# Optimization experiments

Hardware: AMD Instinct MI355X
Metric: run time of the kernel (lower is better)

## Reference

```python
import jax, jax.numpy as jnp
import numpy as np

B, D, H, W_ = 2, 256, 64, 64


def setup_inputs() -> dict:
    key = jax.random.key(0)
    k1, k2 = jax.random.split(key)
    x = jax.random.normal(k1, (B, D, H, W_), dtype=jnp.float32)
    W = jax.random.normal(k2, (3 * D, D), dtype=jnp.float32) * 0.02  # 1x1 conv weight [out,in]
    b = jnp.zeros((3 * D,), dtype=jnp.float32)
    return {"x": x, "W": W, "b": b}


def reference(x, W, b):
    Bs, d, h, w = x.shape
    N = h * w
    sqrtV = d ** 0.25  # sqrt(sqrt(d)); q,k each divided -> qk^T / sqrt(d)
    # 1x1 conv == per-pixel linear over channels
    qkv = jnp.einsum('bchw,oc->bohw', x, W) + b[None, :, None, None]
    q, k, v = jnp.split(qkv, 3, axis=1)
    q = q.reshape(Bs, d, N).transpose(0, 2, 1) / sqrtV  # [B,N,d]
    k = k.reshape(Bs, d, N).transpose(0, 2, 1) / sqrtV
    v = v.reshape(Bs, d, N).transpose(0, 2, 1)
    # Sinkhorn (eps=1, max_iter=1, uniform marginals 1/N), log domain.
    # cost C = -q k^T  =>  -C = q k^T (softmax-style logits)
    negC = jnp.einsum('bnd,bmd->bnm', q, k)  # [B,N,N]
    logm = jnp.log(1.0 / N + 1e-8).astype(x.dtype)
    u = logm - jax.nn.logsumexp(negC, axis=-1)            # [B,N] row update
    vpot = logm - jax.nn.logsumexp(negC + u[..., None], axis=-2)  # [B,N] col update
    pi = jnp.exp(negC + u[..., None] + vpot[:, None, :])  # transport plan = attn
    out = jnp.einsum('bnm,bmd->bnd', pi, v)               # [B,N,d]
    return out.transpose(0, 2, 1).reshape(Bs, d, h, w)
```

## Files before the change

### kernel.cpp

```cpp
#include <hip/hip_runtime.h>
#include <hip/hip_bf16.h>
#include <math.h>

typedef __bf16 bf16;
typedef __bf16 bf16x8 __attribute__((ext_vector_type(8)));
typedef __bf16 bf16x4 __attribute__((ext_vector_type(4)));
typedef float floatx4 __attribute__((ext_vector_type(4)));

typedef const __attribute__((address_space(1))) void* gas_t;
typedef __attribute__((address_space(3))) void* las_t;

#define NPIX 4096
#define DCH 256
#define LSTR 72

#define OFF_XB   ((size_t)0)
#define OFF_WB   ((size_t)4194304)
#define OFF_Q    ((size_t)4587520)
#define OFF_K    ((size_t)8781824)
#define OFF_V    ((size_t)12976128)
#define OFF_E    ((size_t)17170432)
#define OFF_VPP  ((size_t)84279296)
#define OFF_PART ((size_t)88473600)
#define OFF_RS   ((size_t)122028032)
#define OFF_CS   ((size_t)122060800)

__device__ __forceinline__ void stage_tile(const bf16* __restrict__ g0, size_t rstride,
                                           bf16* lds, int t) {
  const int wbase = (t >> 6) << 6;
#pragma unroll
  for (int i = 0; i < 4; i++) {
    int slot = i * 256 + t;
    int row = slot >> 3, seg = slot & 7;
    const bf16* g = g0 + (size_t)row * rstride + ((seg ^ (row & 7)) << 3);
    bf16* l = lds + (size_t)(i * 256 + wbase) * 8;
    __builtin_amdgcn_global_load_lds((gas_t)g, (las_t)l, 16, 0, 0);
  }
}

__global__ __launch_bounds__(256) void transpose_x(
    const float* __restrict__ x, bf16* __restrict__ xb)
{
  __shared__ float ts[64][65];
  const int t = threadIdx.x;
  const int b = blockIdx.z, n0 = blockIdx.x * 64, c0 = blockIdx.y * 64;
  const float* xp = x + ((size_t)b * DCH + c0) * NPIX + n0;
  for (int i = 0; i < 4; i++) {
    int slot = t + i * 256;
    int c = slot >> 4, nq = (slot & 15) * 4;
    float4 v = *(const float4*)(xp + (size_t)c * NPIX + nq);
    ts[c][nq + 0] = v.x; ts[c][nq + 1] = v.y; ts[c][nq + 2] = v.z; ts[c][nq + 3] = v.w;
  }
  __syncthreads();
  for (int i = 0; i < 2; i++) {
    int slot = t + i * 256;
    int n = slot >> 3, cq = (slot & 7) * 8;
    bf16x8 pk;
    for (int j = 0; j < 8; j++) pk[j] = (bf16)ts[cq + j][n];
    *(bf16x8*)(xb + ((size_t)b * NPIX + n0 + n) * DCH + c0 + cq) = pk;
  }
}

__global__ __launch_bounds__(256) void convert_w(
    const float* __restrict__ W, bf16* __restrict__ wb)
{
  size_t i = ((size_t)blockIdx.x * 256 + threadIdx.x) * 4;
  float4 v = *(const float4*)(W + i);
  bf16x4 pk = { (bf16)v.x, (bf16)v.y, (bf16)v.z, (bf16)v.w };
  *(bf16x4*)(wb + i) = pk;
}

__global__ __launch_bounds__(256) void conv_mfma(
    const bf16* __restrict__ xb, const bf16* __restrict__ wb,
    const float* __restrict__ bias,
    bf16* __restrict__ qb, bf16* __restrict__ kb, bf16* __restrict__ vb)
{
  __shared__ bf16 at[128 * 64];
  __shared__ bf16 bt[128 * 64];
  __shared__ float bs[128];
  const int t  = threadIdx.x;
  const int n0 = blockIdx.x * 128;
  const int o0 = blockIdx.y * 128;
  if (t < 128) bs[t] = bias[o0 + t];
  const int lane = t & 63, wave = t >> 6;
  const int wm = wave >> 1, wn = wave & 1;
  const int l15 = lane & 15, quad = lane >> 4;
  const int l7 = l15 & 7;

  floatx4 acc[4][4];
  for (int i=0;i<4;i++) for (int j=0;j<4;j++) for (int r=0;r<4;r++) acc[i][j][r] = 0.f;

  for (int k0 = 0; k0 < DCH; k0 += 64) {
    stage_tile(wb + (size_t)o0 * DCH + k0, DCH, at, t);
    stage_tile(xb + (size_t)n0 * DCH + k0, DCH, bt, t);
    __syncthreads();
    for (int kk = 0; kk < 2; kk++) {
      bf16x8 af[4], bfr[4];
      int sw = ((kk * 4 + quad) ^ l7) * 8;
      for (int f = 0; f < 4; f++)
        af[f]  = *(const bf16x8*)&at[(wm*64 + f*16 + l15)*64 + sw];
      for (int f = 0; f < 4; f++)
        bfr[f] = *(const bf16x8*)&bt[(wn*64 + f*16 + l15)*64 + sw];
      for (int fm = 0; fm < 4; fm++)
        for (int fn = 0; fn < 4; fn++)
          acc[fm][fn] = __builtin_amdgcn_mfma_f32_16x16x32_bf16(af[fm], bfr[fn], acc[fm][fn], 0, 0, 0);
    }
    __syncthreads();
  }

  const float scale = (o0 < 512) ? 0.25f : 1.0f;
  bf16* dst; int od;
  if (o0 < 256)      { dst = qb; od = o0; }
  else if (o0 < 512) { dst = kb; od = o0 - 256; }
  else               { dst = vb; od = o0 - 512; }

  for (int fm = 0; fm < 4; fm++)
    for (int fn = 0; fn < 4; fn++) {
      int o_l = wm*64 + fm*16 + quad*4;
      int n_g = n0 + wn*64 + fn*16 + l15;
      bf16x4 pk;
      for (int r = 0; r < 4; r++)
        pk[r] = (bf16)((acc[fm][fn][r] + bs[o_l + r]) * scale);
      *(bf16x4*)(dst + (size_t)n_g * DCH + od + o_l) = pk;
    }
}

__global__ __launch_bounds__(256) void pass_a(
    const bf16* __restrict__ qb, const bf16* __restrict__ kb,
    bf16* __restrict__ E, float* __restrict__ rowsum)
{
  __shared__ bf16 kt[128 * 64];
  __shared__ bf16 qt[128 * 64];
  __shared__ float rowpart[128];
  const int b = blockIdx.z;
  qb += (size_t)b * NPIX * DCH;
  kb += (size_t)b * NPIX * DCH;
  E  += (size_t)b * NPIX * NPIX;
  rowsum += b * NPIX;
  const int t  = threadIdx.x;
  const int m0 = blockIdx.x * 128;
  const int n0 = blockIdx.y * 128;
  const int lane = t & 63, wave = t >> 6;
  const int wm = wave >> 1, wn = wave & 1;
  const int l15 = lane & 15, quad = lane >> 4;
  const int l7 = l15 & 7;

  floatx4 acc[4][4];
  for (int i=0;i<4;i++) for (int j=0;j<4;j++) for (int r=0;r<4;r++) acc[i][j][r] = 0.f;

  for (int k0 = 0; k0 < DCH; k0 += 64) {
    stage_tile(kb + (size_t)m0 * DCH + k0, DCH, kt, t);
    stage_tile(qb + (size_t)n0 * DCH + k0, DCH, qt, t);
    __syncthreads();
    for (int kk = 0; kk < 2; kk++) {
      bf16x8 af[4], bfr[4];
      int sw = ((kk * 4 + quad) ^ l7) * 8;
      for (int f = 0; f < 4; f++)
        af[f]  = *(const bf16x8*)&kt[(wm*64 + f*16 + l15)*64 + sw];
      for (int f = 0; f < 4; f++)
        bfr[f] = *(const bf16x8*)&qt[(wn*64 + f*16 + l15)*64 + sw];
      for (int fm = 0; fm < 4; fm++)
        for (int fn = 0; fn < 4; fn++)
          acc[fm][fn] = __builtin_amdgcn_mfma_f32_16x16x32_bf16(af[fm], bfr[fn], acc[fm][fn], 0, 0, 0);
    }
    __syncthreads();
  }

  if (t < 128) rowpart[t] = 0.f;
  __syncthreads();

  float rsum[4] = {0.f, 0.f, 0.f, 0.f};
  for (int fm = 0; fm < 4; fm++)
    for (int fn = 0; fn < 4; fn++) {
      int n_g = n0 + wn*64 + fn*16 + l15;
      int m_g = m0 + wm*64 + fm*16 + quad*4;
      bf16x4 pk;
      float s = 0.f;
      for (int r = 0; r < 4; r++) {
        float e = __expf(acc[fm][fn][r]);
        pk[r] = (bf16)e;
        s += e;
      }
      *(bf16x4*)(E + (size_t)n_g * NPIX + m_g) = pk;
      rsum[fn] += s;
    }
  for (int fn = 0; fn < 4; fn++) {
    float s = rsum[fn];
    s += __shfl_xor(s, 16);
    s += __shfl_xor(s, 32);
    if (quad == 0) atomicAdd(&rowpart[wn*64 + fn*16 + l15], s);
  }
  __syncthreads();
  if (t < 128) atomicAdd(&rowsum[n0 + t], rowpart[t]);
}

__global__ __launch_bounds__(256) void col_pass(
    const bf16* __restrict__ E, const float* __restrict__ rowsum,
    float* __restrict__ colsum, float logm)
{
  __shared__ float eus[32];
  const int b = blockIdx.z;
  E += (size_t)b * NPIX * NPIX;
  rowsum += b * NPIX;
  colsum += b * NPIX;
  const int t = threadIdx.x;
  const int col = blockIdx.x * 1024 + t * 4;
  const int nbase = blockIdx.y * 32;
  if (t < 32) eus[t] = __expf(logm - __logf(rowsum[nbase + t]));
  __syncthreads();
  float acc[4] = {0.f, 0.f, 0.f, 0.f};
  for (int r = 0; r < 32; r++) {
    float eu = eus[r];
    bf16x4 ev = *(const bf16x4*)(E + (size_t)(nbase + r) * NPIX + col);
    for (int i = 0; i < 4; i++) acc[i] += eu * (float)ev[i];
  }
  for (int i = 0; i < 4; i++) atomicAdd(&colsum[col + i], acc[i]);
}

__global__ __launch_bounds__(256) void vpp_kernel(
    const bf16* __restrict__ vb, const float* __restrict__ colsum,
    bf16* __restrict__ vppT, float logm)
{
  __shared__ float ts[64][65];
  __shared__ float ef[64];
  const int b = blockIdx.z;
  vb += (size_t)b * NPIX * DCH;
  colsum += b * NPIX;
  vppT += (size_t)b * DCH * NPIX;
  const int t = threadIdx.x;
  const int m0 = blockIdx.x * 64, d0 = blockIdx.y * 64;
  if (t < 64) ef[t] = __expf(logm - __logf(colsum[m0 + t]));
  __syncthreads();
  for (int i = 0; i < 2; i++) {
    int slot = t + i * 256;
    int m = slot >> 3, dq = (slot & 7) * 8;
    bf16x8 v = *(const bf16x8*)(vb + (size_t)(m0 + m) * DCH + d0 + dq);
    float s = ef[m];
    for (int j = 0; j < 8; j++) ts[dq + j][m] = s * (float)v[j];
  }
  __syncthreads();
  for (int i = 0; i < 2; i++) {
    int slot = t + i * 256;
    int d = slot >> 3, mq = (slot & 7) * 8;
    bf16x8 pk;
    for (int j = 0; j < 8; j++) pk[j] = (bf16)ts[d][mq + j];
    *(bf16x8*)(vppT + (size_t)(d0 + d) * NPIX + m0 + mq) = pk;
  }
}

__global__ __launch_bounds__(256) void pass_c(
    const bf16* __restrict__ E, const bf16* __restrict__ vppT,
    const float* __restrict__ rowsum, float* __restrict__ part, float logm)
{
  __shared__ bf16 et[128 * 64];
  __shared__ bf16 vt[128 * 64];
  __shared__ float eus[128];
  const int z = blockIdx.z;
  const int b = z >> 2, kc = z & 3;
  E += (size_t)b * NPIX * NPIX;
  vppT += (size_t)b * DCH * NPIX;
  rowsum += b * NPIX;
  part += (size_t)(b * 4 + kc) * DCH * NPIX;
  const int t  = threadIdx.x;
  const int n0 = blockIdx.x * 128;
  const int d0 = blockIdx.y * 128;
  const int mstart = kc * 1024;
  if (t < 128) eus[t] = __expf(logm - __logf(rowsum[n0 + t]));
  const int lane = t & 63, wave = t >> 6;
  const int wn = wave >> 1, wd = wave & 1;
  const int l15 = lane & 15, quad = lane >> 4;
  const int l7 = l15 & 7;

  floatx4 acc[4][4];
  for (int i=0;i<4;i++) for (int j=0;j<4;j++) for (int r=0;r<4;r++) acc[i][j][r] = 0.f;
  __syncthreads();

  for (int k0 = mstart; k0 < mstart + 1024; k0 += 64) {
    stage_tile(E + (size_t)n0 * NPIX + k0, NPIX, et, t);
    stage_tile(vppT + (size_t)d0 * NPIX + k0, NPIX, vt, t);
    __syncthreads();
    for (int kk = 0; kk < 2; kk++) {
      bf16x8 af[4], bfr[4];
      int sw = ((kk * 4 + quad) ^ l7) * 8;
      for (int f = 0; f < 4; f++)
        af[f]  = *(const bf16x8*)&et[(wn*64 + f*16 + l15)*64 + sw];
      for (int f = 0; f < 4; f++)
        bfr[f] = *(const bf16x8*)&vt[(wd*64 + f*16 + l15)*64 + sw];
      for (int fn = 0; fn < 4; fn++)
        for (int fd = 0; fd < 4; fd++)
          acc[fn][fd] = __builtin_amdgcn_mfma_f32_16x16x32_bf16(af[fn], bfr[fd], acc[fn][fd], 0, 0, 0);
    }
    __syncthreads();
  }

  for (int fn = 0; fn < 4; fn++)
    for (int fd = 0; fd < 4; fd++) {
      int d_g = d0 + wd*64 + fd*16 + l15;
      int n_l = wn*64 + fn*16 + quad*4;
      float4 o;
      o.x = acc[fn][fd][0] * eus[n_l + 0];
      o.y = acc[fn][fd][1] * eus[n_l + 1];
      o.z = acc[fn][fd][2] * eus[n_l + 2];
      o.w = acc[fn][fd][3] * eus[n_l + 3];
      *(float4*)(part + (size_t)d_g * NPIX + n0 + n_l) = o;
    }
}

__global__ __launch_bounds__(256) void reduce_k(
    const float* __restrict__ part, float* __restrict__ outp)
{
  size_t i4 = ((size_t)blockIdx.x * 256 + threadIdx.x) * 4;
  size_t b = i4 >> 20;
  size_t off = i4 & (size_t)1048575;
  const float* p = part + b * 4 * (size_t)1048576 + off;
  float4 a = *(const float4*)(p);
  float4 bq = *(const float4*)(p + (size_t)1048576);
  float4 c = *(const float4*)(p + (size_t)2097152);
  float4 d = *(const float4*)(p + (size_t)3145728);
  float4 s = { a.x+bq.x+c.x+d.x, a.y+bq.y+c.y+d.y, a.z+bq.z+c.z+d.z, a.w+bq.w+c.w+d.w };
  *(float4*)(outp + i4) = s;
}

extern "C" void kernel_launch(void* const* d_in, const int* in_sizes, int n_in,
                              void* d_out, int out_size, void* d_ws, size_t ws_size,
                              hipStream_t stream) {
  (void)in_sizes; (void)n_in; (void)out_size; (void)ws_size;
  const float* x    = (const float*)d_in[0];
  const float* Wm   = (const float*)d_in[1];
  const float* bias = (const float*)d_in[2];
  float* outp = (float*)d_out;
  char* ws = (char*)d_ws;

  bf16*  xb   = (bf16*)(ws + OFF_XB);
  bf16*  wb   = (bf16*)(ws + OFF_WB);
  bf16*  qb   = (bf16*)(ws + OFF_Q);
  bf16*  kb   = (bf16*)(ws + OFF_K);
  bf16*  vb   = (bf16*)(ws + OFF_V);
  bf16*  E    = (bf16*)(ws + OFF_E);
  bf16*  vppT = (bf16*)(ws + OFF_VPP);
  float* part = (float*)(ws + OFF_PART);
  float* rs   = (float*)(ws + OFF_RS);
  float* cs   = (float*)(ws + OFF_CS);

  const float logm = logf(1.0f / 4096.0f + 1e-8f);

  hipMemsetAsync(ws + OFF_RS, 0, 65536, stream);

  transpose_x<<<dim3(64, 4, 2), 256, 0, stream>>>(x, xb);
  convert_w<<<192, 256, 0, stream>>>(Wm, wb);
  conv_mfma<<<dim3(64, 6), 256, 0, stream>>>(xb, wb, bias, qb, kb, vb);

  pass_a<<<dim3(32, 32, 2), 256, 0, stream>>>(qb, kb, E, rs);
  col_pass<<<dim3(4, 128, 2), 256, 0, stream>>>(E, rs, cs, logm);
  vpp_kernel<<<dim3(64, 4, 2), 256, 0, stream>>>(vb, cs, vppT, logm);
  pass_c<<<dim3(32, 2, 8), 256, 0, stream>>>(E, vppT, rs, part, logm);
  reduce_k<<<2048, 256, 0, stream>>>(part, outp);
}
```

Before: 186.4 us.

## Replace global atomics and split-K reduce kernel with partial buffers and output atomics

Merges the x transpose and W conversion into one prep kernel. Row and column sums are no longer accumulated with global atomics: each pass_a block and each col_pass block writes its own partial vector, and consumers sum the 32 partials when they need them. The separate reduce kernel and its partial buffer are removed; pass_c instead atomically adds its split-K contributions straight into a zeroed output. This removes one launch, the part-buffer round trip and atomic contention on rowsum and colsum. In exchange it adds redundant partial-sum reads in three kernels, a full output memset, per-element float atomics in pass_c, and a summation order that is no longer fixed.

```diff
diff --git a/kernel.cpp b/kernel.cpp
--- a/kernel.cpp
+++ b/kernel.cpp
@@ -5,6 +5,7 @@
 typedef __bf16 bf16;
 typedef __bf16 bf16x8 __attribute__((ext_vector_type(8)));
 typedef __bf16 bf16x4 __attribute__((ext_vector_type(4)));
+typedef __bf16 bf16x2 __attribute__((ext_vector_type(2)));
 typedef float floatx4 __attribute__((ext_vector_type(4)));
 
 typedef const __attribute__((address_space(1))) void* gas_t;
@@ -12,7 +13,6 @@
 
 #define NPIX 4096
 #define DCH 256
-#define LSTR 72
 
 #define OFF_XB   ((size_t)0)
 #define OFF_WB   ((size_t)4194304)
@@ -21,9 +21,8 @@
 #define OFF_V    ((size_t)12976128)
 #define OFF_E    ((size_t)17170432)
 #define OFF_VPP  ((size_t)84279296)
-#define OFF_PART ((size_t)88473600)
-#define OFF_RS   ((size_t)122028032)
-#define OFF_CS   ((size_t)122060800)
+#define OFF_RP   ((size_t)88473600)
+#define OFF_CP   ((size_t)89522176)
 
 __device__ __forceinline__ void stage_tile(const bf16* __restrict__ g0, size_t rstride,
                                            bf16* lds, int t) {
@@ -38,11 +37,21 @@
   }
 }
 
-__global__ __launch_bounds__(256) void transpose_x(
-    const float* __restrict__ x, bf16* __restrict__ xb)
-{
+__global__ __launch_bounds__(256) void prep(
+    const float* __restrict__ x, const float* __restrict__ W,
+    bf16* __restrict__ xb, bf16* __restrict__ wb)
+{
+  const int t = threadIdx.x;
+  if (blockIdx.y == 4) {
+    int gid = (blockIdx.z * 64 + blockIdx.x) * 256 + t;
+    for (int i = gid; i < 49152; i += 32768) {
+      float4 v = *(const float4*)(W + (size_t)i * 4);
+      bf16x4 pk = { (bf16)v.x, (bf16)v.y, (bf16)v.z, (bf16)v.w };
+      *(bf16x4*)(wb + (size_t)i * 4) = pk;
+    }
+    return;
+  }
   __shared__ float ts[64][65];
-  const int t = threadIdx.x;
   const int b = blockIdx.z, n0 = blockIdx.x * 64, c0 = blockIdx.y * 64;
   const float* xp = x + ((size_t)b * DCH + c0) * NPIX + n0;
   for (int i = 0; i < 4; i++) {
@@ -59,15 +68,6 @@
     for (int j = 0; j < 8; j++) pk[j] = (bf16)ts[cq + j][n];
     *(bf16x8*)(xb + ((size_t)b * NPIX + n0 + n) * DCH + c0 + cq) = pk;
   }
-}
-
-__global__ __launch_bounds__(256) void convert_w(
-    const float* __restrict__ W, bf16* __restrict__ wb)
-{
-  size_t i = ((size_t)blockIdx.x * 256 + threadIdx.x) * 4;
-  float4 v = *(const float4*)(W + i);
-  bf16x4 pk = { (bf16)v.x, (bf16)v.y, (bf16)v.z, (bf16)v.w };
-  *(bf16x4*)(wb + i) = pk;
 }
 
 __global__ __launch_bounds__(256) void conv_mfma(
@@ -127,7 +127,7 @@
 
 __global__ __launch_bounds__(256) void pass_a(
     const bf16* __restrict__ qb, const bf16* __restrict__ kb,
-    bf16* __restrict__ E, float* __restrict__ rowsum)
+    bf16* __restrict__ E, float* __restrict__ rowpartG)
 {
   __shared__ bf16 kt[128 * 64];
   __shared__ bf16 qt[128 * 64];
@@ -136,7 +136,7 @@
   qb += (size_t)b * NPIX * DCH;
   kb += (size_t)b * NPIX * DCH;
   E  += (size_t)b * NPIX * NPIX;
-  rowsum += b * NPIX;
+  float* rp = rowpartG + ((size_t)b * 32 + blockIdx.x) * NPIX;
   const int t  = threadIdx.x;
   const int m0 = blockIdx.x * 128;
   const int n0 = blockIdx.y * 128;
@@ -191,45 +191,54 @@
     if (quad == 0) atomicAdd(&rowpart[wn*64 + fn*16 + l15], s);
   }
   __syncthreads();
-  if (t < 128) atomicAdd(&rowsum[n0 + t], rowpart[t]);
+  if (t < 128) rp[n0 + t] = rowpart[t];
 }
 
 __global__ __launch_bounds__(256) void col_pass(
-    const bf16* __restrict__ E, const float* __restrict__ rowsum,
-    float* __restrict__ colsum, float logm)
-{
-  __shared__ float eus[32];
+    const bf16* __restrict__ E, const float* __restrict__ rowpartG,
+    float* __restrict__ colpartG, float logm)
+{
+  __shared__ float eus[128];
   const int b = blockIdx.z;
   E += (size_t)b * NPIX * NPIX;
-  rowsum += b * NPIX;
-  colsum += b * NPIX;
+  const float* rp = rowpartG + (size_t)b * 32 * NPIX;
+  float* cp = colpartG + ((size_t)b * 32 + blockIdx.y) * NPIX;
   const int t = threadIdx.x;
-  const int col = blockIdx.x * 1024 + t * 4;
-  const int nbase = blockIdx.y * 32;
-  if (t < 32) eus[t] = __expf(logm - __logf(rowsum[nbase + t]));
-  __syncthreads();
-  float acc[4] = {0.f, 0.f, 0.f, 0.f};
-  for (int r = 0; r < 32; r++) {
+  const int col = blockIdx.x * 512 + t * 2;
+  const int nbase = blockIdx.y * 128;
+  if (t < 128) {
+    float s = 0.f;
+    for (int mi = 0; mi < 32; mi++) s += rp[(size_t)mi * NPIX + nbase + t];
+    eus[t] = __expf(logm - __logf(s));
+  }
+  __syncthreads();
+  float a0 = 0.f, a1 = 0.f;
+  for (int r = 0; r < 128; r++) {
     float eu = eus[r];
-    bf16x4 ev = *(const bf16x4*)(E + (size_t)(nbase + r) * NPIX + col);
-    for (int i = 0; i < 4; i++) acc[i] += eu * (float)ev[i];
-  }
-  for (int i = 0; i < 4; i++) atomicAdd(&colsum[col + i], acc[i]);
+    bf16x2 ev = *(const bf16x2*)(E + (size_t)(nbase + r) * NPIX + col);
+    a0 += eu * (float)ev[0];
+    a1 += eu * (float)ev[1];
+  }
+  cp[col] = a0; cp[col + 1] = a1;
 }
 
 __global__ __launch_bounds__(256) void vpp_kernel(
-    const bf16* __restrict__ vb, const float* __restrict__ colsum,
+    const bf16* __restrict__ vb, const float* __restrict__ colpartG,
     bf16* __restrict__ vppT, float logm)
 {
   __shared__ float ts[64][65];
   __shared__ float ef[64];
   const int b = blockIdx.z;
   vb += (size_t)b * NPIX * DCH;
-  colsum += b * NPIX;
+  const float* cp = colpartG + (size_t)b * 32 * NPIX;
   vppT += (size_t)b * DCH * NPIX;
   const int t = threadIdx.x;
   const int m0 = blockIdx.x * 64, d0 = blockIdx.y * 64;
-  if (t < 64) ef[t] = __expf(logm - __logf(colsum[m0 + t]));
+  if (t < 64) {
+    float s = 0.f;
+    for (int g = 0; g < 32; g++) s += cp[(size_t)g * NPIX + m0 + t];
+    ef[t] = __expf(logm - __logf(s));
+  }
   __syncthreads();
   for (int i = 0; i < 2; i++) {
     int slot = t + i * 256;
@@ -250,7 +259,7 @@
 
 __global__ __launch_bounds__(256) void pass_c(
     const bf16* __restrict__ E, const bf16* __restrict__ vppT,
-    const float* __restrict__ rowsum, float* __restrict__ part, float logm)
+    const float* __restrict__ rowpartG, float* __restrict__ outp, float logm)
 {
   __shared__ bf16 et[128 * 64];
   __shared__ bf16 vt[128 * 64];
@@ -259,13 +268,17 @@
   const int b = z >> 2, kc = z & 3;
   E += (size_t)b * NPIX * NPIX;
   vppT += (size_t)b * DCH * NPIX;
-  rowsum += b * NPIX;
-  part += (size_t)(b * 4 + kc) * DCH * NPIX;
+  const float* rp = rowpartG + (size_t)b * 32 * NPIX;
+  outp += (size_t)b * DCH * NPIX;
   const int t  = threadIdx.x;
   const int n0 = blockIdx.x * 128;
   const int d0 = blockIdx.y * 128;
   const int mstart = kc * 1024;
-  if (t < 128) eus[t] = __expf(logm - __logf(rowsum[n0 + t]));
+  if (t < 128) {
+    float s = 0.f;
+    for (int mi = 0; mi < 32; mi++) s += rp[(size_t)mi * NPIX + n0 + t];
+    eus[t] = __expf(logm - __logf(s));
+  }
   const int lane = t & 63, wave = t >> 6;
   const int wn = wave >> 1, wd = wave & 1;
   const int l15 = lane & 15, quad = lane >> 4;
@@ -297,28 +310,11 @@
     for (int fd = 0; fd < 4; fd++) {
       int d_g = d0 + wd*64 + fd*16 + l15;
       int n_l = wn*64 + fn*16 + quad*4;
-      float4 o;
-      o.x = acc[fn][fd][0] * eus[n_l + 0];
-      o.y = acc[fn][fd][1] * eus[n_l + 1];
-      o.z = acc[fn][fd][2] * eus[n_l + 2];
-      o.w = acc[fn][fd][3] * eus[n_l + 3];
-      *(float4*)(part + (size_t)d_g * NPIX + n0 + n_l) = o;
-    }
-}
-
-__global__ __launch_bounds__(256) void reduce_k(
-    const float* __restrict__ part, float* __restrict__ outp)
-{
-  size_t i4 = ((size_t)blockIdx.x * 256 + threadIdx.x) * 4;
-  size_t b = i4 >> 20;
-  size_t off = i4 & (size_t)1048575;
-  const float* p = part + b * 4 * (size_t)1048576 + off;
-  float4 a = *(const float4*)(p);
-  float4 bq = *(const float4*)(p + (size_t)1048576);
-  float4 c = *(const float4*)(p + (size_t)2097152);
-  float4 d = *(const float4*)(p + (size_t)3145728);
-  float4 s = { a.x+bq.x+c.x+d.x, a.y+bq.y+c.y+d.y, a.z+bq.z+c.z+d.z, a.w+bq.w+c.w+d.w };
-  *(float4*)(outp + i4) = s;
+      float* op = outp + (size_t)d_g * NPIX + n0 + n_l;
+#pragma unroll
+      for (int r = 0; r < 4; r++)
+        atomicAdd(op + r, acc[fn][fd][r] * eus[n_l + r]);
+    }
 }
 
 extern "C" void kernel_launch(void* const* d_in, const int* in_sizes, int n_in,
@@ -338,21 +334,18 @@
   bf16*  vb   = (bf16*)(ws + OFF_V);
   bf16*  E    = (bf16*)(ws + OFF_E);
   bf16*  vppT = (bf16*)(ws + OFF_VPP);
-  float* part = (float*)(ws + OFF_PART);
-  float* rs   = (float*)(ws + OFF_RS);
-  float* cs   = (float*)(ws + OFF_CS);
+  float* rp   = (float*)(ws + OFF_RP);
+  float* cp   = (float*)(ws + OFF_CP);
 
   const float logm = logf(1.0f / 4096.0f + 1e-8f);
 
-  hipMemsetAsync(ws + OFF_RS, 0, 65536, stream);
-
-  transpose_x<<<dim3(64, 4, 2), 256, 0, stream>>>(x, xb);
-  convert_w<<<192, 256, 0, stream>>>(Wm, wb);
+  hipMemsetAsync(outp, 0, (size_t)2 * DCH * NPIX * sizeof(float), stream);
+
+  prep<<<dim3(64, 5, 2), 256, 0, stream>>>(x, Wm, xb, wb);
   conv_mfma<<<dim3(64, 6), 256, 0, stream>>>(xb, wb, bias, qb, kb, vb);
 
-  pass_a<<<dim3(32, 32, 2), 256, 0, stream>>>(qb, kb, E, rs);
-  col_pass<<<dim3(4, 128, 2), 256, 0, stream>>>(E, rs, cs, logm);
-  vpp_kernel<<<dim3(64, 4, 2), 256, 0, stream>>>(vb, cs, vppT, logm);
-  pass_c<<<dim3(32, 2, 8), 256, 0, stream>>>(E, vppT, rs, part, logm);
-  reduce_k<<<2048, 256, 0, stream>>>(part, outp);
-}
+  pass_a<<<dim3(32, 32, 2), 256, 0, stream>>>(qb, kb, E, rp);
+  col_pass<<<dim3(8, 32, 2), 256, 0, stream>>>(E, rp, cp, logm);
+  vpp_kernel<<<dim3(64, 4, 2), 256, 0, stream>>>(vb, cp, vppT, logm);
+  pass_c<<<dim3(32, 2, 8), 256, 0, stream>>>(E, vppT, rp, outp, logm);
+}
```

Result: slower. 247.3 us (+32.7%).
